# Performance work log

Hardware: AMD Instinct MI355X
Metric: run time of the kernel (lower is better)

Reference implementation:

```python
import jax, jax.numpy as jnp
import numpy as np


def setup_inputs() -> dict:
    key = jax.random.key(0)
    k1, k2 = jax.random.split(key)
    B, TOTAL_BITS, H, W = 16, 64, 128, 128
    C_OUT, N_BITS = 64, 4
    # binary bit-plane input, values in {0, 1}
    x = (jax.random.uniform(k1, (B, TOTAL_BITS, H, W)) < 0.5).astype(jnp.float32)
    # random bit-selection map: which input bit feeds each (out_channel, bit_pos)
    rp_map = jax.random.randint(k2, (C_OUT, N_BITS), 0, TOTAL_BITS)
    return {"x": x, "rp_map": rp_map}


def reference(x, rp_map):
    # bit_select_mode path of RPLayer.forward:
    #   gather n_bits_per_out random bits per output channel, then
    #   bit-pack with power-of-two weights (MAC-free projection).
    B, TB, H, W = x.shape
    C, nb = rp_map.shape
    # [B, TB, H, W] -> [B*H*W, TB]
    x_flat = x.transpose(0, 2, 3, 1).reshape(B * H * W, TB)
    # gather: [B*H*W, C, nb]  (fancy-index along bit axis, no expand needed)
    gathered = x_flat[:, rp_map]
    # power-of-two pack weights [1, 2, 4, 8, ...]
    pack_w = 2.0 ** jnp.arange(nb, dtype=x.dtype)
    packed = jnp.einsum('ncb,b->nc', gathered, pack_w)  # [B*H*W, C]
    # [B, H, W, C] -> [B, C, H, W]
    return packed.reshape(B, H, W, C).transpose(0, 3, 1, 2)
```

## Files before the change

### kernel.cpp

```cpp
#include <hip/hip_runtime.h>
#include <cstdint>
#include <cstddef>

constexpr int Bn = 16;
constexpr int TBn = 64;
constexpr int Hn = 128;
constexpr int Wn = 128;
constexpr int Cn = 64;
constexpr int HW = Hn * Wn;
constexpr int TOTAL_PIX = Bn * HW;
constexpr int PIX_PER_BLOCK = 256;
constexpr int BLOCKS = TOTAL_PIX / PIX_PER_BLOCK;
constexpr int BLOCKS_PER_IMG = HW / PIX_PER_BLOCK;
constexpr int MROW = 20;

__global__ __launch_bounds__(256) void rp_pack_lds(
    const float* __restrict__ x,
    const int* __restrict__ rp,
    float* __restrict__ out)
{
    __shared__ int4 s_rp[Cn];
    __shared__ unsigned short m16[64 * MROW];

    if (threadIdx.x < Cn) {
        s_rp[threadIdx.x] = reinterpret_cast<const int4*>(rp)[threadIdx.x];
    }

    const int b = blockIdx.x >> 6;
    const int pix0 = (blockIdx.x & 63) << 8;
    const int g = threadIdx.x & 63;
    const int q = threadIdx.x >> 6;

    const float* xb = x + (size_t)b * TBn * HW + (size_t)(q * 16) * HW + pix0 + g * 4;

    uint32_t p0 = 0, p1 = 0, p2 = 0, p3 = 0;
    #pragma unroll
    for (int i = 0; i < 16; ++i) {
        const float4 v = *reinterpret_cast<const float4*>(xb + (size_t)i * HW);
        p0 |= ((__float_as_uint(v.x) >> 23) & 1u) << i;
        p1 |= ((__float_as_uint(v.y) >> 23) & 1u) << i;
        p2 |= ((__float_as_uint(v.z) >> 23) & 1u) << i;
        p3 |= ((__float_as_uint(v.w) >> 23) & 1u) << i;
    }

    unsigned short* row = &m16[g * MROW];
    row[0 * 4 + q] = (unsigned short)p0;
    row[1 * 4 + q] = (unsigned short)p1;
    row[2 * 4 + q] = (unsigned short)p2;
    row[3 * 4 + q] = (unsigned short)p3;

    __syncthreads();

    const uint64_t m0 = *reinterpret_cast<const uint64_t*>(&row[0]);
    const uint64_t m1 = *reinterpret_cast<const uint64_t*>(&row[4]);
    const uint64_t m2 = *reinterpret_cast<const uint64_t*>(&row[8]);
    const uint64_t m3 = *reinterpret_cast<const uint64_t*>(&row[12]);

    const int c0 = q * 16;
    float* ob = out + (size_t)b * Cn * HW + (size_t)c0 * HW + pix0 + g * 4;

    #pragma unroll
    for (int ci = 0; ci < 16; ++ci) {
        const int4 r = s_rp[c0 + ci];
        const unsigned i0 = (unsigned)r.x;
        const unsigned i1 = (unsigned)r.y;
        const unsigned i2 = (unsigned)r.z;
        const unsigned i3 = (unsigned)r.w;

        float4 o;
        o.x = (float)((unsigned)((m0 >> i0) & 1ull)
                    | ((unsigned)((m0 >> i1) & 1ull) << 1)
                    | ((unsigned)((m0 >> i2) & 1ull) << 2)
                    | ((unsigned)((m0 >> i3) & 1ull) << 3));
        o.y = (float)((unsigned)((m1 >> i0) & 1ull)
                    | ((unsigned)((m1 >> i1) & 1ull) << 1)
                    | ((unsigned)((m1 >> i2) & 1ull) << 2)
                    | ((unsigned)((m1 >> i3) & 1ull) << 3));
        o.z = (float)((unsigned)((m2 >> i0) & 1ull)
                    | ((unsigned)((m2 >> i1) & 1ull) << 1)
                    | ((unsigned)((m2 >> i2) & 1ull) << 2)
                    | ((unsigned)((m2 >> i3) & 1ull) << 3));
        o.w = (float)((unsigned)((m3 >> i0) & 1ull)
                    | ((unsigned)((m3 >> i1) & 1ull) << 1)
                    | ((unsigned)((m3 >> i2) & 1ull) << 2)
                    | ((unsigned)((m3 >> i3) & 1ull) << 3));

        *reinterpret_cast<float4*>(ob + (size_t)ci * HW) = o;
    }
}

extern "C" void kernel_launch(void* const* d_in, const int* in_sizes, int n_in,
                              void* d_out, int out_size, void* d_ws, size_t ws_size,
                              hipStream_t stream) {
    const float* x = (const float*)d_in[0];
    const int* rp = (const int*)d_in[1];
    float* out = (float*)d_out;

    constexpr int BLOCK = 256;
    rp_pack_lds<<<BLOCKS, BLOCK, 0, stream>>>(x, rp, out);
}
```

Before: 26.46 us.

## Split work into 8 bit-groups per 128-pixel block to raise parallelism

Each block now covers 128 pixels with 8 warps-of-32 threads, and each thread loads 8 bit planes instead of 16 and writes 8 output channels. The four per-pixel byte masks are packed into one 32-bit LDS word and unpacked into 64-bit masks after the barrier, and the launch bounds now request 8 blocks per CU. The goal is more blocks and fewer serial loads per thread, for better latency hiding on a memory-bound kernel, at the cost of extra LDS reads and unpack ALU work per thread.

```diff
diff --git a/kernel.cpp b/kernel.cpp
--- a/kernel.cpp
+++ b/kernel.cpp
@@ -9,83 +9,87 @@
 constexpr int Cn = 64;
 constexpr int HW = Hn * Wn;
 constexpr int TOTAL_PIX = Bn * HW;
-constexpr int PIX_PER_BLOCK = 256;
+constexpr int PIX_PER_BLOCK = 128;
 constexpr int BLOCKS = TOTAL_PIX / PIX_PER_BLOCK;
 constexpr int BLOCKS_PER_IMG = HW / PIX_PER_BLOCK;
-constexpr int MROW = 20;
+constexpr int MROW_DW = 10;
 
-__global__ __launch_bounds__(256) void rp_pack_lds(
+__global__ __launch_bounds__(256, 8) void rp_pack_lds8(
     const float* __restrict__ x,
     const int* __restrict__ rp,
     float* __restrict__ out)
 {
     __shared__ int4 s_rp[Cn];
-    __shared__ unsigned short m16[64 * MROW];
+    __shared__ uint32_t m32[32 * MROW_DW];
 
     if (threadIdx.x < Cn) {
         s_rp[threadIdx.x] = reinterpret_cast<const int4*>(rp)[threadIdx.x];
     }
 
-    const int b = blockIdx.x >> 6;
-    const int pix0 = (blockIdx.x & 63) << 8;
-    const int g = threadIdx.x & 63;
-    const int q = threadIdx.x >> 6;
+    const int b = blockIdx.x >> 7;
+    const int pix0 = (blockIdx.x & 127) << 7;
+    const int g = threadIdx.x & 31;
+    const int o = threadIdx.x >> 5;
 
-    const float* xb = x + (size_t)b * TBn * HW + (size_t)(q * 16) * HW + pix0 + g * 4;
+    const float* xb = x + (size_t)b * TBn * HW + (size_t)(o * 8) * HW + pix0 + g * 4;
 
     uint32_t p0 = 0, p1 = 0, p2 = 0, p3 = 0;
     #pragma unroll
-    for (int i = 0; i < 16; ++i) {
+    for (int i = 0; i < 8; ++i) {
         const float4 v = *reinterpret_cast<const float4*>(xb + (size_t)i * HW);
         p0 |= ((__float_as_uint(v.x) >> 23) & 1u) << i;
         p1 |= ((__float_as_uint(v.y) >> 23) & 1u) << i;
         p2 |= ((__float_as_uint(v.z) >> 23) & 1u) << i;
         p3 |= ((__float_as_uint(v.w) >> 23) & 1u) << i;
     }
-
-    unsigned short* row = &m16[g * MROW];
-    row[0 * 4 + q] = (unsigned short)p0;
-    row[1 * 4 + q] = (unsigned short)p1;
-    row[2 * 4 + q] = (unsigned short)p2;
-    row[3 * 4 + q] = (unsigned short)p3;
+    m32[g * MROW_DW + o] = p0 | (p1 << 8) | (p2 << 16) | (p3 << 24);
 
     __syncthreads();
 
-    const uint64_t m0 = *reinterpret_cast<const uint64_t*>(&row[0]);
-    const uint64_t m1 = *reinterpret_cast<const uint64_t*>(&row[4]);
-    const uint64_t m2 = *reinterpret_cast<const uint64_t*>(&row[8]);
-    const uint64_t m3 = *reinterpret_cast<const uint64_t*>(&row[12]);
+    uint32_t r[8];
+    #pragma unroll
+    for (int i = 0; i < 8; ++i) {
+        r[i] = m32[g * MROW_DW + i];
+    }
+    uint64_t m0 = 0, m1 = 0, m2 = 0, m3 = 0;
+    #pragma unroll
+    for (int i = 0; i < 8; ++i) {
+        m0 |= (uint64_t)((r[i]      ) & 0xffu) << (i * 8);
+        m1 |= (uint64_t)((r[i] >>  8) & 0xffu) << (i * 8);
+        m2 |= (uint64_t)((r[i] >> 16) & 0xffu) << (i * 8);
+        m3 |= (uint64_t)((r[i] >> 24) & 0xffu) << (i * 8);
+    }
 
-    const int c0 = q * 16;
+    const int c0 = o * 8;
     float* ob = out + (size_t)b * Cn * HW + (size_t)c0 * HW + pix0 + g * 4;
 
     #pragma unroll
-    for (int ci = 0; ci < 16; ++ci) {
-        const int4 r = s_rp[c0 + ci];
-        const unsigned i0 = (unsigned)r.x;
-        const unsigned i1 = (unsigned)r.y;
-        const unsigned i2 = (unsigned)r.z;
-        const unsigned i3 = (unsigned)r.w;
+    for (int ci = 0; ci < 8; ++ci) {
+        const int4 rr = s_rp[c0 + ci];
+        const unsigned i0 = (unsigned)rr.x;
+        const unsigned i1 = (unsigned)rr.y;
+        const unsigned i2 = (unsigned)rr.z;
+        const unsigned i3 = (unsigned)rr.w;
 
-        float4 o;
-        o.x = (float)((unsigned)((m0 >> i0) & 1ull)
-                    | ((unsigned)((m0 >> i1) & 1ull) << 1)
-                    | ((unsigned)((m0 >> i2) & 1ull) << 2)
-                    | ((unsigned)((m0 >> i3) & 1ull) << 3));
-        o.y = (float)((unsigned)((m1 >> i0) & 1ull)
-                    | ((unsigned)((m1 >> i1) & 1ull) << 1)
-                    | ((unsigned)((m1 >> i2) & 1ull) << 2)
-                    | ((unsigned)((m1 >> i3) & 1ull) << 3));
-        o.z = (float)((unsigned)((m2 >> i0) & 1ull)
-                    | ((unsigned)((m2 >> i1) & 1ull) << 1)
-                    | ((unsigned)((m2 >> i2) & 1ull) << 2)
-                    | ((unsigned)((m2 >> i3) & 1ull) << 3));
-        o.w = (float)((unsigned)((m3 >> i0) & 1ull)
-                    | ((unsigned)((m3 >> i1) & 1ull) << 1)
-                    | ((unsigned)((m3 >> i2) & 1ull) << 2)
-                    | ((unsigned)((m3 >> i3) & 1ull) << 3));
+        float4 oo;
+        oo.x = (float)((unsigned)((m0 >> i0) & 1ull)
+                     | ((unsigned)((m0 >> i1) & 1ull) << 1)
+                     | ((unsigned)((m0 >> i2) & 1ull) << 2)
+                     | ((unsigned)((m0 >> i3) & 1ull) << 3));
+        oo.y = (float)((unsigned)((m1 >> i0) & 1ull)
+                     | ((unsigned)((m1 >> i1) & 1ull) << 1)
+                     | ((unsigned)((m1 >> i2) & 1ull) << 2)
+                     | ((unsigned)((m1 >> i3) & 1ull) << 3));
+        oo.z = (float)((unsigned)((m2 >> i0) & 1ull)
+                     | ((unsigned)((m2 >> i1) & 1ull) << 1)
+                     | ((unsigned)((m2 >> i2) & 1ull) << 2)
+                     | ((unsigned)((m2 >> i3) & 1ull) << 3));
+        oo.w = (float)((unsigned)((m3 >> i0) & 1ull)
+                     | ((unsigned)((m3 >> i1) & 1ull) << 1)
+                     | ((unsigned)((m3 >> i2) & 1ull) << 2)
+                     | ((unsigned)((m3 >> i3) & 1ull) << 3));
 
-        *reinterpret_cast<float4*>(ob + (size_t)ci * HW) = o;
+        *reinterpret_cast<float4*>(ob + (size_t)ci * HW) = oo;
     }
 }
 
@@ -97,5 +101,5 @@
     float* out = (float*)d_out;
 
     constexpr int BLOCK = 256;
-    rp_pack_lds<<<BLOCKS, BLOCK, 0, stream>>>(x, rp, out);
+    rp_pack_lds8<<<BLOCKS, BLOCK, 0, stream>>>(x, rp, out);
 }
```

Result: slower. 27.52 us (+4.0%).
